# Kernel optimization log

Hardware: AMD Instinct MI355X
Metric: run time of the kernel (lower is better)

The kernel has to match this reference:

```python
import jax, jax.numpy as jnp
import numpy as np

M, T, NX, U = 256, 512, 256, 256


def setup_inputs() -> dict:
    key = jax.random.key(0)
    ks = jax.random.split(key, 8)
    u = lambda k, s: jax.random.uniform(k, s, dtype=jnp.float32) * 0.01
    return {
        "x": jax.random.normal(ks[0], (M, T, NX), dtype=jnp.float32),
        "a0": jax.random.normal(ks[1], (M, U), dtype=jnp.float32),
        "wcx": u(ks[2], (NX, U)),
        "wcc": u(ks[3], (U, U)),
        "bc": jnp.zeros((1, U), jnp.float32),
        "wux": u(ks[4], (NX, U)),
        "wuc": u(ks[5], (U, U)),
        "bu": jnp.zeros((1, U), jnp.float32),
        "wrx": u(ks[6], (NX, U)),
        "wrc": u(ks[7], (U, U)),
        "br": jnp.zeros((1, U), jnp.float32),
    }


def reference(x, a0, wcx, wcc, bc, wux, wuc, bu, wrx, wrc, br):
    # x: [m, t, nx] -> scan over time; state c: [m, units]
    def step(c, xt):
        g_u = jax.nn.sigmoid(c @ wuc + xt @ wux + bu)
        g_r = jax.nn.sigmoid(c @ wrc + xt @ wrx + br)
        # NB: original is (g_r * c_prev) @ wcc due to operator precedence
        cand = jnp.tanh((g_r * c) @ wcc + xt @ wcx + bc)
        c_new = g_u * cand + (1.0 - g_u) * c
        return c_new, None

    c_final, _ = jax.lax.scan(step, a0, jnp.swapaxes(x, 0, 1))
    # return_sequences=False, return_state=False -> last hidden state [m, units]
    return c_final
```

## Files before the change

### kernel.cpp

```cpp
#include <hip/hip_runtime.h>

typedef _Float16 h2 __attribute__((ext_vector_type(2)));
typedef _Float16 h4 __attribute__((ext_vector_type(4)));
typedef _Float16 h8 __attribute__((ext_vector_type(8)));
typedef float f4v __attribute__((ext_vector_type(4)));

#define U_DIM 256
#define M_DIM 256
#define T_DIM 512

#if defined(__has_builtin)
#if __has_builtin(__builtin_amdgcn_fdot2)
#define HAVE_FDOT2 1
#endif
#endif

__device__ __forceinline__ float fdot2f(h2 a, h2 b, float c) {
#ifdef HAVE_FDOT2
  return __builtin_amdgcn_fdot2(a, b, c, false);
#else
  return fmaf((float)a[0], (float)b[0], fmaf((float)a[1], (float)b[1], c));
#endif
}

__device__ __forceinline__ float fast_sigmoid(float z) {
  return __builtin_amdgcn_rcpf(1.f + __expf(-z));
}
__device__ __forceinline__ float fast_tanh(float z) {
  return fmaf(2.f, __builtin_amdgcn_rcpf(1.f + __expf(-2.f * z)), -1.f);
}

template <int CTRL>
__device__ __forceinline__ float dpp_xadd(float x) {
  int y = __builtin_amdgcn_update_dpp(0, __float_as_int(x), CTRL, 0xF, 0xF, true);
  return x + __int_as_float(y);
}
__device__ __forceinline__ float reduce8(float x) {
  x = dpp_xadd<0xB1>(x);
  x = dpp_xadd<0x4E>(x);
  x = dpp_xadd<0x141>(x);
  return x;
}

__global__ void conv_x(const float* __restrict__ x, h8* __restrict__ x16, int n8) {
  int i = blockIdx.x * 256 + threadIdx.x;
  if (i >= n8) return;
  const float4* p = (const float4*)(x + (size_t)i * 8);
  float4 v0 = p[0], v1 = p[1];
  h8 o = {(_Float16)v0.x, (_Float16)v0.y, (_Float16)v0.z, (_Float16)v0.w,
          (_Float16)v1.x, (_Float16)v1.y, (_Float16)v1.z, (_Float16)v1.w};
  x16[i] = o;
}

__global__ void prep_xw(const float* __restrict__ wux, const float* __restrict__ wrx,
                        const float* __restrict__ wcx, h8* __restrict__ wt16) {
  int idx = blockIdx.x * 256 + threadIdx.x;
  int mtx = idx >> 13;
  int rem = idx & 8191;
  int n = rem >> 5;
  int kv = rem & 31;
  const float* W = (mtx == 0) ? wux : ((mtx == 1) ? wrx : wcx);
  h8 o;
#pragma unroll
  for (int e = 0; e < 8; ++e) o[e] = (_Float16)W[(size_t)(kv * 8 + e) * U_DIM + n];
  wt16[idx] = o;
}

__global__ void prep_w(const float* __restrict__ wuc, const float* __restrict__ wrc,
                       const float* __restrict__ wcc, h8* __restrict__ w16) {
  int idx = blockIdx.x * 256 + threadIdx.x;
  int mtx = idx >> 13;
  int rem = idx & 8191;
  int tid = rem >> 4;
  int q   = rem & 15;
  int o = q >> 2, v = q & 3;
  int g = tid >> 3, s = tid & 7;
  const float* W = (mtx == 0) ? wuc : ((mtx == 1) ? wrc : wcc);
  int col = 4 * g + o;
  int k0 = 32 * s + 8 * v;
  h8 out;
#pragma unroll
  for (int e = 0; e < 8; ++e) out[e] = (_Float16)W[(size_t)(k0 + e) * U_DIM + col];
  w16[idx] = out;
}

__global__ __launch_bounds__(256, 2)
void xproj_mfma(const h8* __restrict__ x16, const h8* __restrict__ wt16,
                const float* __restrict__ Bu, const float* __restrict__ Br,
                const float* __restrict__ Bc,
                _Float16* __restrict__ XU, _Float16* __restrict__ XR,
                _Float16* __restrict__ XC, int t0, int len) {
  const int mtx = blockIdx.z;
  const float* Bv = (mtx == 0) ? Bu : ((mtx == 1) ? Br : Bc);
  _Float16* O = (mtx == 0) ? XU : ((mtx == 1) ? XR : XC);
  const h8* W = wt16 + (size_t)mtx * 256 * 32;

  __shared__ _Float16 a_sh[128][40];
  __shared__ _Float16 b_sh[128][40];

  const int tid = threadIdx.x;
  const int r0 = blockIdx.x * 128;
  const int c0 = blockIdx.y * 128;

  const int srow = tid >> 1;
  const int spart = tid & 1;
  const int r = r0 + srow;
  const int mm = r / len;
  const int tc = r - mm * len;
  const h8* arow = x16 + ((size_t)mm * T_DIM + (size_t)(t0 + tc)) * 32;
  const h8* brow = W + (size_t)(c0 + srow) * 32;

  const int lane = tid & 63;
  const int w = tid >> 6;
  const int quad = lane >> 4;
  const int mrow = lane & 15;

  f4v acc[2][8];
#pragma unroll
  for (int fr = 0; fr < 2; ++fr)
#pragma unroll
    for (int fc = 0; fc < 8; ++fc) acc[fr][fc] = f4v{0.f, 0.f, 0.f, 0.f};

  for (int k8 = 0; k8 < 32; k8 += 4) {
    h8 a0 = arow[k8 + 2 * spart];
    h8 a1 = arow[k8 + 2 * spart + 1];
    h8 b0 = brow[k8 + 2 * spart];
    h8 b1 = brow[k8 + 2 * spart + 1];
    __syncthreads();
    *(h8*)&a_sh[srow][spart * 16]     = a0;
    *(h8*)&a_sh[srow][spart * 16 + 8] = a1;
    *(h8*)&b_sh[srow][spart * 16]     = b0;
    *(h8*)&b_sh[srow][spart * 16 + 8] = b1;
    __syncthreads();
    h8 af0 = *(const h8*)&a_sh[32 * w + mrow][quad * 8];
    h8 af1 = *(const h8*)&a_sh[32 * w + 16 + mrow][quad * 8];
#pragma unroll
    for (int fc = 0; fc < 8; ++fc) {
      h8 bf = *(const h8*)&b_sh[fc * 16 + mrow][quad * 8];
      acc[0][fc] = __builtin_amdgcn_mfma_f32_16x16x32_f16(af0, bf, acc[0][fc], 0, 0, 0);
      acc[1][fc] = __builtin_amdgcn_mfma_f32_16x16x32_f16(af1, bf, acc[1][fc], 0, 0, 0);
    }
  }

#pragma unroll
  for (int fc = 0; fc < 8; ++fc) {
    int col = c0 + fc * 16 + mrow;
    float bb = Bv[col];
#pragma unroll
    for (int fr = 0; fr < 2; ++fr)
#pragma unroll
      for (int reg = 0; reg < 4; ++reg) {
        int rr = r0 + 32 * w + fr * 16 + quad * 4 + reg;
        O[(size_t)rr * U_DIM + col] = (_Float16)(acc[fr][fc][reg] + bb);
      }
  }
}

__global__ __launch_bounds__(512, 1)
void gru_rec(const _Float16* __restrict__ XU, const _Float16* __restrict__ XR,
             const _Float16* __restrict__ XC, const h8* __restrict__ w16,
             const float* __restrict__ c_in, float* __restrict__ c_out, int len) {
  const int m = blockIdx.x;
  const int tid = threadIdx.x;
  const int g = tid >> 3;
  const int s = tid & 7;
  const int so = s & 3;
  const int cb = 5 * s;
  const int j = 4 * g + so;
  const int hwj = 40 * (j >> 5) + (j & 31);
  const bool wr_lane = (s < 4);

  __shared__ h8 ch8[40];
  __shared__ h8 hh8[40];
  _Float16* cwp = (_Float16*)ch8;
  _Float16* hwp = (_Float16*)hh8;

  const h8* wub = w16 + (size_t)tid * 16;
  const h8* wrb = wub + 8192;
  const h8* wcb = wub + 16384;

#define DECL_W(l) h8 wu##l = wub[l]; h8 wr##l = wrb[l]; h8 wc##l = wcb[l];
  DECL_W(0)  DECL_W(1)  DECL_W(2)  DECL_W(3)
  DECL_W(4)  DECL_W(5)  DECL_W(6)  DECL_W(7)
  DECL_W(8)  DECL_W(9)  DECL_W(10) DECL_W(11)
  DECL_W(12) DECL_W(13) DECL_W(14) DECL_W(15)
#undef DECL_W

  float cj = c_in[m * U_DIM + j];
  if (wr_lane) cwp[hwj] = (_Float16)cj;

  const _Float16* XUb = XU + (size_t)m * len * U_DIM;
  const _Float16* XRb = XR + (size_t)m * len * U_DIM;
  const _Float16* XCb = XC + (size_t)m * len * U_DIM;

  int off = j;
  float xuv = (float)XUb[off], xrv = (float)XRb[off], xcv = (float)XCb[off];

  __syncthreads();

#define P1O(cv, l, o)                                                     \
  pu##o = fdot2f(h2{cv[0], cv[1]}, h2{wu##l[0], wu##l[1]}, pu##o);        \
  pu##o = fdot2f(h2{cv[2], cv[3]}, h2{wu##l[2], wu##l[3]}, pu##o);        \
  pu##o = fdot2f(h2{cv[4], cv[5]}, h2{wu##l[4], wu##l[5]}, pu##o);        \
  pu##o = fdot2f(h2{cv[6], cv[7]}, h2{wu##l[6], wu##l[7]}, pu##o);        \
  pr##o = fdot2f(h2{cv[0], cv[1]}, h2{wr##l[0], wr##l[1]}, pr##o);        \
  pr##o = fdot2f(h2{cv[2], cv[3]}, h2{wr##l[2], wr##l[3]}, pr##o);        \
  pr##o = fdot2f(h2{cv[4], cv[5]}, h2{wr##l[4], wr##l[5]}, pr##o);        \
  pr##o = fdot2f(h2{cv[6], cv[7]}, h2{wr##l[6], wr##l[7]}, pr##o);
#define PASS1V(v, la, lb, lc, ld) { h8 cv = ch8[cb + v];                  \
  P1O(cv, la, 0) P1O(cv, lb, 1) P1O(cv, lc, 2) P1O(cv, ld, 3) }

#define P2O(hv, l, o)                                                     \
  pc##o = fdot2f(h2{hv[0], hv[1]}, h2{wc##l[0], wc##l[1]}, pc##o);        \
  pc##o = fdot2f(h2{hv[2], hv[3]}, h2{wc##l[2], wc##l[3]}, pc##o);        \
  pc##o = fdot2f(h2{hv[4], hv[5]}, h2{wc##l[4], wc##l[5]}, pc##o);        \
  pc##o = fdot2f(h2{hv[6], hv[7]}, h2{wc##l[6], wc##l[7]}, pc##o);
#define PASS2V(v, la, lb, lc, ld) { h8 hv = hh8[cb + v];                  \
  P2O(hv, la, 0) P2O(hv, lb, 1) P2O(hv, lc, 2) P2O(hv, ld, 3) }

  for (int t = 0; t < len; ++t) {
    int offn = off + ((t + 1 < len) ? U_DIM : 0);
    float nxu = (float)XUb[offn], nxr = (float)XRb[offn], nxc = (float)XCb[offn];

    float pu0 = 0.f, pu1 = 0.f, pu2 = 0.f, pu3 = 0.f;
    float pr0 = 0.f, pr1 = 0.f, pr2 = 0.f, pr3 = 0.f;
    PASS1V(0, 0, 4, 8, 12)
    PASS1V(1, 1, 5, 9, 13)
    PASS1V(2, 2, 6, 10, 14)
    PASS1V(3, 3, 7, 11, 15)

    pu0 = reduce8(pu0); pu1 = reduce8(pu1); pu2 = reduce8(pu2); pu3 = reduce8(pu3);
    pr0 = reduce8(pr0); pr1 = reduce8(pr1); pr2 = reduce8(pr2); pr3 = reduce8(pr3);

    float puj = (so & 2) ? ((so & 1) ? pu3 : pu2) : ((so & 1) ? pu1 : pu0);
    float prj = (so & 2) ? ((so & 1) ? pr3 : pr2) : ((so & 1) ? pr1 : pr0);
    float gu = fast_sigmoid(puj + xuv);
    float gr = fast_sigmoid(prj + xrv);
    if (wr_lane) hwp[hwj] = (_Float16)(gr * cj);
    __syncthreads();

    float pc0 = 0.f, pc1 = 0.f, pc2 = 0.f, pc3 = 0.f;
    PASS2V(0, 0, 4, 8, 12)
    PASS2V(1, 1, 5, 9, 13)
    PASS2V(2, 2, 6, 10, 14)
    PASS2V(3, 3, 7, 11, 15)

    pc0 = reduce8(pc0); pc1 = reduce8(pc1); pc2 = reduce8(pc2); pc3 = reduce8(pc3);
    float pcj = (so & 2) ? ((so & 1) ? pc3 : pc2) : ((so & 1) ? pc1 : pc0);

    float cand = fast_tanh(pcj + xcv);
    cj = fmaf(gu, cand - cj, cj);
    if (wr_lane) cwp[hwj] = (_Float16)cj;

    xuv = nxu; xrv = nxr; xcv = nxc; off = offn;
    __syncthreads();
  }

#undef P1O
#undef PASS1V
#undef P2O
#undef PASS2V

  if (wr_lane) c_out[m * U_DIM + j] = cj;
}

extern "C" void kernel_launch(void* const* d_in, const int* in_sizes, int n_in,
                              void* d_out, int out_size, void* d_ws, size_t ws_size,
                              hipStream_t stream) {
  const float* x   = (const float*)d_in[0];
  const float* a0  = (const float*)d_in[1];
  const float* wcx = (const float*)d_in[2];
  const float* wcc = (const float*)d_in[3];
  const float* bc  = (const float*)d_in[4];
  const float* wux = (const float*)d_in[5];
  const float* wuc = (const float*)d_in[6];
  const float* bu  = (const float*)d_in[7];
  const float* wrx = (const float*)d_in[8];
  const float* wrc = (const float*)d_in[9];
  const float* br  = (const float*)d_in[10];
  float* out = (float*)d_out;

  const size_t x16_bytes = (size_t)M_DIM * T_DIM * U_DIM * 2;
  const size_t wt_bytes  = 3ull * 256 * 32 * 16;
  const size_t w16_bytes = 3ull * 512 * 16 * 16;
  const size_t fixed = x16_bytes + wt_bytes + w16_bytes;

  h8* x16  = (h8*)d_ws;
  h8* wt16 = (h8*)((char*)d_ws + x16_bytes);
  h8* w16  = (h8*)((char*)d_ws + x16_bytes + wt_bytes);
  _Float16* XU0 = (_Float16*)((char*)d_ws + fixed);

  size_t avail = (ws_size > fixed) ? (ws_size - fixed) : 0;
  const size_t perT = 3ull * M_DIM * U_DIM * 2;
  int Tc = (int)(avail / perT);
  if (Tc > T_DIM) Tc = T_DIM;
  if (Tc < 1) Tc = 1;
  int nch = (T_DIM + Tc - 1) / Tc;
  Tc = (T_DIM + nch - 1) / nch;

  _Float16* XU = XU0;
  _Float16* XR = XU + (size_t)M_DIM * Tc * U_DIM;
  _Float16* XC = XR + (size_t)M_DIM * Tc * U_DIM;

  conv_x<<<16384, 256, 0, stream>>>(x, x16, M_DIM * T_DIM * U_DIM / 8);
  prep_xw<<<96, 256, 0, stream>>>(wux, wrx, wcx, wt16);
  prep_w<<<96, 256, 0, stream>>>(wuc, wrc, wcc, w16);

  for (int t0 = 0; t0 < T_DIM; t0 += Tc) {
    int lenc = (T_DIM - t0) < Tc ? (T_DIM - t0) : Tc;
    dim3 g((M_DIM * lenc) / 128, 2, 3);
    xproj_mfma<<<g, 256, 0, stream>>>(x16, wt16, bu, br, bc,
                                      XU, XR, XC, t0, lenc);
    gru_rec<<<M_DIM, 512, 0, stream>>>(XU, XR, XC, w16,
                                       (t0 == 0 ? a0 : out), out, lenc);
  }
}
```

Baseline: 964.4 us.

## Double recurrent block to 1024 threads with two output columns per group

The recurrence kernel now runs 1024 threads per batch row. Each 8-lane group computes 2 output units instead of 4, so every thread holds half as many fp16 weight vectors in registers and does half the dot-product work per step. The weight prep kernel is re-laid out to match, and the x-projection values are loaded as packed half2 pairs. This shortens the per-timestep serial chain, at the cost of more waves taking part in each block barrier, and it may change register allocation under the new launch bounds.

```diff
diff --git a/kernel.cpp b/kernel.cpp
--- a/kernel.cpp
+++ b/kernel.cpp
@@ -1,7 +1,6 @@
 #include <hip/hip_runtime.h>
 
 typedef _Float16 h2 __attribute__((ext_vector_type(2)));
-typedef _Float16 h4 __attribute__((ext_vector_type(4)));
 typedef _Float16 h8 __attribute__((ext_vector_type(8)));
 typedef float f4v __attribute__((ext_vector_type(4)));
 
@@ -71,12 +70,12 @@
   int idx = blockIdx.x * 256 + threadIdx.x;
   int mtx = idx >> 13;
   int rem = idx & 8191;
-  int tid = rem >> 4;
-  int q   = rem & 15;
+  int tid = rem >> 3;
+  int q   = rem & 7;
   int o = q >> 2, v = q & 3;
   int g = tid >> 3, s = tid & 7;
   const float* W = (mtx == 0) ? wuc : ((mtx == 1) ? wrc : wcc);
-  int col = 4 * g + o;
+  int col = 2 * g + o;
   int k0 = 32 * s + 8 * v;
   h8 out;
 #pragma unroll
@@ -156,7 +155,7 @@
   }
 }
 
-__global__ __launch_bounds__(512, 1)
+__global__ __launch_bounds__(1024)
 void gru_rec(const _Float16* __restrict__ XU, const _Float16* __restrict__ XR,
              const _Float16* __restrict__ XC, const h8* __restrict__ w16,
              const float* __restrict__ c_in, float* __restrict__ c_out, int len) {
@@ -164,104 +163,98 @@
   const int tid = threadIdx.x;
   const int g = tid >> 3;
   const int s = tid & 7;
-  const int so = s & 3;
   const int cb = 5 * s;
-  const int j = 4 * g + so;
-  const int hwj = 40 * (j >> 5) + (j & 31);
-  const bool wr_lane = (s < 4);
+  const int j0 = 2 * g;
+  const int hw = (5 * (j0 >> 5) + ((j0 & 31) >> 3)) * 8 + (j0 & 7);
+  const bool wr = (s == 0);
 
   __shared__ h8 ch8[40];
   __shared__ h8 hh8[40];
   _Float16* cwp = (_Float16*)ch8;
   _Float16* hwp = (_Float16*)hh8;
 
-  const h8* wub = w16 + (size_t)tid * 16;
+  const h8* wub = w16 + (size_t)tid * 8;
   const h8* wrb = wub + 8192;
   const h8* wcb = wub + 16384;
 
 #define DECL_W(l) h8 wu##l = wub[l]; h8 wr##l = wrb[l]; h8 wc##l = wcb[l];
   DECL_W(0)  DECL_W(1)  DECL_W(2)  DECL_W(3)
   DECL_W(4)  DECL_W(5)  DECL_W(6)  DECL_W(7)
-  DECL_W(8)  DECL_W(9)  DECL_W(10) DECL_W(11)
-  DECL_W(12) DECL_W(13) DECL_W(14) DECL_W(15)
 #undef DECL_W
 
-  float cj = c_in[m * U_DIM + j];
-  if (wr_lane) cwp[hwj] = (_Float16)cj;
-
-  const _Float16* XUb = XU + (size_t)m * len * U_DIM;
-  const _Float16* XRb = XR + (size_t)m * len * U_DIM;
-  const _Float16* XCb = XC + (size_t)m * len * U_DIM;
-
-  int off = j;
-  float xuv = (float)XUb[off], xrv = (float)XRb[off], xcv = (float)XCb[off];
+  float2 cc = *(const float2*)(c_in + m * U_DIM + j0);
+  float cj0 = cc.x, cj1 = cc.y;
+  if (wr) *(h2*)(cwp + hw) = h2{(_Float16)cj0, (_Float16)cj1};
+
+  const char* pU = (const char*)(XU + (size_t)m * len * U_DIM) + 4 * g;
+  const char* pR = (const char*)(XR + (size_t)m * len * U_DIM) + 4 * g;
+  const char* pC = (const char*)(XC + (size_t)m * len * U_DIM) + 4 * g;
+
+  int off = 0;
+  h2 vu = *(const h2*)(pU + off);
+  h2 vr = *(const h2*)(pR + off);
+  h2 vc = *(const h2*)(pC + off);
 
   __syncthreads();
 
-#define P1O(cv, l, o)                                                     \
-  pu##o = fdot2f(h2{cv[0], cv[1]}, h2{wu##l[0], wu##l[1]}, pu##o);        \
-  pu##o = fdot2f(h2{cv[2], cv[3]}, h2{wu##l[2], wu##l[3]}, pu##o);        \
-  pu##o = fdot2f(h2{cv[4], cv[5]}, h2{wu##l[4], wu##l[5]}, pu##o);        \
-  pu##o = fdot2f(h2{cv[6], cv[7]}, h2{wu##l[6], wu##l[7]}, pu##o);        \
-  pr##o = fdot2f(h2{cv[0], cv[1]}, h2{wr##l[0], wr##l[1]}, pr##o);        \
-  pr##o = fdot2f(h2{cv[2], cv[3]}, h2{wr##l[2], wr##l[3]}, pr##o);        \
-  pr##o = fdot2f(h2{cv[4], cv[5]}, h2{wr##l[4], wr##l[5]}, pr##o);        \
-  pr##o = fdot2f(h2{cv[6], cv[7]}, h2{wr##l[6], wr##l[7]}, pr##o);
-#define PASS1V(v, la, lb, lc, ld) { h8 cv = ch8[cb + v];                  \
-  P1O(cv, la, 0) P1O(cv, lb, 1) P1O(cv, lc, 2) P1O(cv, ld, 3) }
-
-#define P2O(hv, l, o)                                                     \
-  pc##o = fdot2f(h2{hv[0], hv[1]}, h2{wc##l[0], wc##l[1]}, pc##o);        \
-  pc##o = fdot2f(h2{hv[2], hv[3]}, h2{wc##l[2], wc##l[3]}, pc##o);        \
-  pc##o = fdot2f(h2{hv[4], hv[5]}, h2{wc##l[4], wc##l[5]}, pc##o);        \
-  pc##o = fdot2f(h2{hv[6], hv[7]}, h2{wc##l[6], wc##l[7]}, pc##o);
-#define PASS2V(v, la, lb, lc, ld) { h8 hv = hh8[cb + v];                  \
-  P2O(hv, la, 0) P2O(hv, lb, 1) P2O(hv, lc, 2) P2O(hv, ld, 3) }
+#define DOT8(acc, cv, w)                                                  \
+  acc = fdot2f(h2{cv[0], cv[1]}, h2{w[0], w[1]}, acc);                    \
+  acc = fdot2f(h2{cv[2], cv[3]}, h2{w[2], w[3]}, acc);                    \
+  acc = fdot2f(h2{cv[4], cv[5]}, h2{w[4], w[5]}, acc);                    \
+  acc = fdot2f(h2{cv[6], cv[7]}, h2{w[6], w[7]}, acc);
+
+#define PASS1V(v, a, b) { h8 cv = ch8[cb + v];                            \
+  DOT8(pu0, cv, wu##a) DOT8(pu1, cv, wu##b)                               \
+  DOT8(pr0, cv, wr##a) DOT8(pr1, cv, wr##b) }
+
+#define PASS2V(v, a, b) { h8 hv = hh8[cb + v];                            \
+  DOT8(pc0, hv, wc##a) DOT8(pc1, hv, wc##b) }
 
   for (int t = 0; t < len; ++t) {
-    int offn = off + ((t + 1 < len) ? U_DIM : 0);
-    float nxu = (float)XUb[offn], nxr = (float)XRb[offn], nxc = (float)XCb[offn];
-
-    float pu0 = 0.f, pu1 = 0.f, pu2 = 0.f, pu3 = 0.f;
-    float pr0 = 0.f, pr1 = 0.f, pr2 = 0.f, pr3 = 0.f;
-    PASS1V(0, 0, 4, 8, 12)
-    PASS1V(1, 1, 5, 9, 13)
-    PASS1V(2, 2, 6, 10, 14)
-    PASS1V(3, 3, 7, 11, 15)
-
-    pu0 = reduce8(pu0); pu1 = reduce8(pu1); pu2 = reduce8(pu2); pu3 = reduce8(pu3);
-    pr0 = reduce8(pr0); pr1 = reduce8(pr1); pr2 = reduce8(pr2); pr3 = reduce8(pr3);
-
-    float puj = (so & 2) ? ((so & 1) ? pu3 : pu2) : ((so & 1) ? pu1 : pu0);
-    float prj = (so & 2) ? ((so & 1) ? pr3 : pr2) : ((so & 1) ? pr1 : pr0);
-    float gu = fast_sigmoid(puj + xuv);
-    float gr = fast_sigmoid(prj + xrv);
-    if (wr_lane) hwp[hwj] = (_Float16)(gr * cj);
+    int offn = off + ((t + 1 < len) ? (U_DIM * 2) : 0);
+    h2 nu = *(const h2*)(pU + offn);
+    h2 nr = *(const h2*)(pR + offn);
+    h2 nc = *(const h2*)(pC + offn);
+
+    float pu0 = 0.f, pu1 = 0.f, pr0 = 0.f, pr1 = 0.f;
+    PASS1V(0, 0, 4)
+    PASS1V(1, 1, 5)
+    PASS1V(2, 2, 6)
+    PASS1V(3, 3, 7)
+
+    pu0 = reduce8(pu0); pu1 = reduce8(pu1);
+    pr0 = reduce8(pr0); pr1 = reduce8(pr1);
+
+    float gu0 = fast_sigmoid(pu0 + (float)vu[0]);
+    float gu1 = fast_sigmoid(pu1 + (float)vu[1]);
+    float gr0 = fast_sigmoid(pr0 + (float)vr[0]);
+    float gr1 = fast_sigmoid(pr1 + (float)vr[1]);
+    if (wr) *(h2*)(hwp + hw) = h2{(_Float16)(gr0 * cj0), (_Float16)(gr1 * cj1)};
     __syncthreads();
 
-    float pc0 = 0.f, pc1 = 0.f, pc2 = 0.f, pc3 = 0.f;
-    PASS2V(0, 0, 4, 8, 12)
-    PASS2V(1, 1, 5, 9, 13)
-    PASS2V(2, 2, 6, 10, 14)
-    PASS2V(3, 3, 7, 11, 15)
-
-    pc0 = reduce8(pc0); pc1 = reduce8(pc1); pc2 = reduce8(pc2); pc3 = reduce8(pc3);
-    float pcj = (so & 2) ? ((so & 1) ? pc3 : pc2) : ((so & 1) ? pc1 : pc0);
-
-    float cand = fast_tanh(pcj + xcv);
-    cj = fmaf(gu, cand - cj, cj);
-    if (wr_lane) cwp[hwj] = (_Float16)cj;
-
-    xuv = nxu; xrv = nxr; xcv = nxc; off = offn;
+    float pc0 = 0.f, pc1 = 0.f;
+    PASS2V(0, 0, 4)
+    PASS2V(1, 1, 5)
+    PASS2V(2, 2, 6)
+    PASS2V(3, 3, 7)
+
+    pc0 = reduce8(pc0); pc1 = reduce8(pc1);
+
+    float cd0 = fast_tanh(pc0 + (float)vc[0]);
+    float cd1 = fast_tanh(pc1 + (float)vc[1]);
+    cj0 = fmaf(gu0, cd0 - cj0, cj0);
+    cj1 = fmaf(gu1, cd1 - cj1, cj1);
+    if (wr) *(h2*)(cwp + hw) = h2{(_Float16)cj0, (_Float16)cj1};
+
+    vu = nu; vr = nr; vc = nc; off = offn;
     __syncthreads();
   }
 
-#undef P1O
+#undef DOT8
 #undef PASS1V
-#undef P2O
 #undef PASS2V
 
-  if (wr_lane) c_out[m * U_DIM + j] = cj;
+  if (wr) *(float2*)(c_out + m * U_DIM + j0) = float2{cj0, cj1};
 }
 
 extern "C" void kernel_launch(void* const* d_in, const int* in_sizes, int n_in,
@@ -282,7 +275,7 @@
 
   const size_t x16_bytes = (size_t)M_DIM * T_DIM * U_DIM * 2;
   const size_t wt_bytes  = 3ull * 256 * 32 * 16;
-  const size_t w16_bytes = 3ull * 512 * 16 * 16;
+  const size_t w16_bytes = 3ull * 1024 * 8 * 16;
   const size_t fixed = x16_bytes + wt_bytes + w16_bytes;
 
   h8* x16  = (h8*)d_ws;
@@ -311,7 +304,7 @@
     dim3 g((M_DIM * lenc) / 128, 2, 3);
     xproj_mfma<<<g, 256, 0, stream>>>(x16, wt16, bu, br, bc,
                                       XU, XR, XC, t0, lenc);
-    gru_rec<<<M_DIM, 512, 0, stream>>>(XU, XR, XC, w16,
-                                       (t0 == 0 ? a0 : out), out, lenc);
+    gru_rec<<<M_DIM, 1024, 0, stream>>>(XU, XR, XC, w16,
+                                        (t0 == 0 ? a0 : out), out, lenc);
   }
 }
```

Measured after the change: 1.462 ms. 51.6% more time.
